# Optimization experiments

Hardware: AMD Instinct MI355X
Metric: run time of the kernel (lower is better)

The kernel has to match this reference:

```python
import jax, jax.numpy as jnp
import numpy as np

N, E, C, S = 30000, 480000, 256, 4
T_EVO = 0.1        # evolution_time
MAX_EIG = 0.5      # max_eigenval in create_ultra_stable_hamiltonian
MAX_NORM = 0.01    # max_norm in ultra_stable_matrix_exp
MAX_TERMS = 4
LN_EPS = 1e-5


def _build_subgraphs(edge_index, n, s):
    """Emulates the per-node k_hop=1 BFS (capped at max_subgraph_size=s) and the
    subgraph laplacian Hamiltonian build (edge_weight=0.1, self-loops added).
    Pure structural preprocessing: integer/constant w.r.t. all float params."""
    src = np.asarray(edge_index[0], dtype=np.int64)
    dst = np.asarray(edge_index[1], dtype=np.int64)
    loops = np.arange(n, dtype=np.int64)
    src = np.concatenate([src, loops]); dst = np.concatenate([dst, loops])
    order = np.argsort(src, kind='stable')
    src_s, dst_s = src[order], dst[order]
    starts = np.searchsorted(src_s, np.arange(n))
    ends = np.searchsorted(src_s, np.arange(n) + 1)
    edge_set = set((src * n + dst).tolist())
    sub_nodes = np.zeros((n, s), dtype=np.int64)
    sub_mask = np.zeros((n, s), dtype=np.float32)
    H = np.zeros((n, s, s), dtype=np.float32)
    for i in range(n):
        nbrs = [i]
        for d in dst_s[starts[i]:ends[i]]:
            d = int(d)
            if d != i and d not in nbrs:
                nbrs.append(d)
                if len(nbrs) == s:
                    break
        m = len(nbrs)
        sub_nodes[i, :m] = nbrs
        sub_nodes[i, m:] = i          # pad with center (masked out below)
        sub_mask[i, :m] = 1.0
        A = np.zeros((s, s), dtype=np.float32)
        for a in range(m):
            ka = nbrs[a] * n
            for b in range(m):
                if (ka + nbrs[b]) in edge_set:
                    A[a, b] = 1.0
        deg = np.maximum(A.sum(axis=1), 1e-6)   # degree(row), clamped like torch
        H[i] = np.diag(deg) - 0.1 * A           # laplacian with edge_weight=0.1
    return sub_nodes, sub_mask, H


def _mat_fro(M):
    return jnp.sqrt(jnp.sum(jnp.abs(M) ** 2, axis=(-2, -1)))


def _unitary_from_H(sub_H):
    """ultra_stable_matrix_exp, batched over N tiny [S,S] Hamiltonians.
    The torch .item() norm/eigenvalue rescales detach gradients, so treating this
    whole block as parameter-independent (it is: H is structural) is faithful."""
    Hc = sub_H.astype(jnp.complex64)
    ev = jnp.linalg.eigvals(Hc)                              # [N,S] (CPU op)
    mx = jnp.max(ev.real, axis=-1)
    Hc = Hc * jnp.where(mx > MAX_EIG, MAX_EIG / mx, 1.0)[:, None, None]
    hn = _mat_fro(Hc)
    Hc = Hc * jnp.where(hn > MAX_NORM, MAX_NORM / hn, 1.0)[:, None, None]
    A = (-1j) * Hc * (T_EVO * 0.1)                           # scaled_H
    I = jnp.eye(S, dtype=jnp.complex64)
    U = jnp.broadcast_to(I, Hc.shape)
    term = U
    for k in range(1, MAX_TERMS + 1):
        term = jnp.matmul(term, A) / k
        tn = _mat_fro(term)
        term = term * jnp.where(tn > 0.1, 0.1 / tn, 1.0)[:, None, None]
        U = U + term
    err = _mat_fro(jnp.matmul(U, jnp.conj(jnp.swapaxes(U, -1, -2))) - I)
    U = jnp.where((err > 0.1)[:, None, None], I + A * 0.01, U)
    return U


def _cplx_linear(xr, xi, wr, wi, br, bi):
    xr = jnp.clip(xr, -10.0, 10.0); xi = jnp.clip(xi, -10.0, 10.0)
    re = xr @ wr.T - xi @ wi.T + br
    im = xr @ wi.T + xi @ wr.T + bi
    return re + 1j * im


def _cln(z, w, b, eps=LN_EPS):
    # UltraStableComplexLayerNorm, training-mode batch stats over dim 0
    mag = jnp.clip(jnp.sqrt(z.real ** 2 + z.imag ** 2 + eps), eps, 1000.0)
    mean = mag.mean(0)
    var = mag.var(0)
    nm = (mag - mean) / (jnp.sqrt(var + eps) + eps)
    sm = jnp.clip(nm * jnp.abs(w) + b, eps, 10.0)
    ph = jnp.arctan2(jnp.clip(z.imag, -1e6, 1e6), jnp.clip(z.real, -1e6, 1e6) + 1e-10)
    return sm * jnp.cos(ph) + 1j * (sm * jnp.sin(ph))


def _crelu(z, leak=0.01, mx=5.0):
    r = jnp.clip(z.real, -mx, mx); i = jnp.clip(z.imag, -mx, mx)
    return jnp.where(r > 0, r, leak * r) + 1j * jnp.where(i > 0, i, leak * i)


def setup_inputs() -> dict:
    key = jax.random.key(0)
    k1, k2, k3, k4 = jax.random.split(key, 4)
    x = jax.random.normal(k1, (N, C), dtype=jnp.float32)
    edge_index = jax.random.randint(k2, (2, E), 0, N, dtype=jnp.int64)
    sub_nodes, sub_mask, sub_H = _build_subgraphs(np.asarray(edge_index), N, S)
    std = np.sqrt(0.5 / C).astype(np.float32)
    w_real = jax.random.normal(k3, (C, C), dtype=jnp.float32) * std
    w_imag = jax.random.normal(k4, (C, C), dtype=jnp.float32) * std
    return {
        'x': x,
        'edge_index': edge_index,
        'sub_nodes': jnp.asarray(sub_nodes),
        'sub_mask': jnp.asarray(sub_mask),
        'sub_H': jnp.asarray(sub_H),
        'w_real': w_real,
        'w_imag': w_imag,
        'b_real': jnp.zeros((C,), jnp.float32),
        'b_imag': jnp.zeros((C,), jnp.float32),
        'ln_weight': jnp.full((C,), 0.1, jnp.float32),
        'ln_bias': jnp.zeros((C,), jnp.float32),
        'evolution_scale': jnp.asarray(0.1, jnp.float32),
    }


def reference(x, edge_index, sub_nodes, sub_mask, sub_H,
              w_real, w_imag, b_real, b_imag, ln_weight, ln_bias,
              evolution_scale):
    # complex linear (input is real -> imag part zero, matching torch.complex(x, 0*x))
    h = _cplx_linear(x, jnp.zeros_like(x), w_real, w_imag, b_real, b_imag)  # [N,C] c64
    U = _unitary_from_H(sub_H)                                              # [N,S,S]
    sub_x = h[sub_nodes] * sub_mask[..., None]                              # [N,S,C]
    # center node is slot 0 of each subgraph -> take row 0 of U @ sub_x
    evolved = jnp.einsum('ns,nsc->nc', U[:, 0, :], sub_x)
    out = evolved * evolution_scale + x.astype(jnp.complex64)  # residual (in==out)
    out = _cln(out, ln_weight, ln_bias)
    out = _crelu(out)
    # dropout is eval-mode identity
    return jnp.concatenate([out.real, out.imag], axis=-1)      # [N, 2C] float32
```

## Files before the change

kernel.cpp:

```cpp
#include <hip/hip_runtime.h>
#include <stdint.h>

#define N_NODES 30000
#define NC 256

typedef _Float16 f16x8 __attribute__((ext_vector_type(8)));
typedef _Float16 f16x4 __attribute__((ext_vector_type(4)));
typedef _Float16 f16x2 __attribute__((ext_vector_type(2)));
typedef float f32x4 __attribute__((ext_vector_type(4)));

#define NBX 7500
#define NBW 128
#define NBP 118
__global__ __launch_bounds__(256) void k_pre(
    const float* __restrict__ x, _Float16* __restrict__ xb,
    const float* __restrict__ wr, const float* __restrict__ wi,
    _Float16* __restrict__ Wb,
    const float* __restrict__ subH, const float* __restrict__ sub_mask,
    const float* __restrict__ escp, float* __restrict__ c4,
    float* __restrict__ ssum, float* __restrict__ ssumsq)
{
    int bid = blockIdx.x, tid = threadIdx.x;
    if (bid < NBX) {
        int i = (bid * 256 + tid) * 4;
        float4 v = *reinterpret_cast<const float4*>(x + i);
        f16x4 o;
        o[0] = (_Float16)fminf(fmaxf(v.x, -10.f), 10.f);
        o[1] = (_Float16)fminf(fmaxf(v.y, -10.f), 10.f);
        o[2] = (_Float16)fminf(fmaxf(v.z, -10.f), 10.f);
        o[3] = (_Float16)fminf(fmaxf(v.w, -10.f), 10.f);
        *reinterpret_cast<f16x4*>(xb + i) = o;
    } else if (bid < NBX + NBW) {
        int i = ((bid - NBX) * 256 + tid) * 4;
        const float* src = (i < NC * NC) ? (wr + i) : (wi + (i - NC * NC));
        float4 v = *reinterpret_cast<const float4*>(src);
        f16x4 o;
        o[0] = (_Float16)v.x; o[1] = (_Float16)v.y;
        o[2] = (_Float16)v.z; o[3] = (_Float16)v.w;
        *reinterpret_cast<f16x4*>(Wb + i) = o;
    } else if (bid < NBX + NBW + NBP) {
        int node = (bid - NBX - NBW) * 256 + tid;
        if (node < N_NODES) {
            float esc = *escp;
            const float4* Hp = reinterpret_cast<const float4*>(subH + node * 16);
            float4 r0 = Hp[0], r1 = Hp[1], r2 = Hp[2], r3 = Hp[3];
            float fr = r0.x * r0.x + r0.y * r0.y + r0.z * r0.z + r0.w * r0.w
                     + r1.x * r1.x + r1.y * r1.y + r1.z * r1.z + r1.w * r1.w
                     + r2.x * r2.x + r2.y * r2.y + r2.z * r2.z + r2.w * r2.w
                     + r3.x * r3.x + r3.y * r3.y + r3.z * r3.z + r3.w * r3.w;
            float coef = 1e-4f * rsqrtf(fr) * esc;
            float4 m = *reinterpret_cast<const float4*>(sub_mask + node * 4);
            float4 o;
            o.x = coef * r0.x * m.x;
            o.y = coef * r0.y * m.y;
            o.z = coef * r0.z * m.z;
            o.w = coef * r0.w * m.w;
            *reinterpret_cast<float4*>(c4 + node * 4) = o;
        }
    } else {
        ssum[tid] = 0.f;
        ssumsq[tid] = 0.f;
    }
}

__global__ __launch_bounds__(256, 2) void k_gemm(
    const _Float16* __restrict__ A, const _Float16* __restrict__ B,
    const float* __restrict__ br, const float* __restrict__ bi,
    _Float16* __restrict__ H)
{
    int bid = blockIdx.x;
    int bm = bid >> 1, cs = bid & 1;
    int tid = threadIdx.x;
    int lane = tid & 63, wave = tid >> 6;
    int quad = lane >> 4, l16 = lane & 15;
    int wm = wave >> 1, wn = wave & 1;
    int row0 = bm * 128 + wm * 64;

    f16x8 af[4][8];
#pragma unroll
    for (int mi = 0; mi < 4; mi++) {
        int r = row0 + mi * 16 + l16;
        if (r >= N_NODES) r = N_NODES - 1;
        const _Float16* ap = A + r * NC + quad * 8;
#pragma unroll
        for (int kc = 0; kc < 8; kc++)
            af[mi][kc] = *reinterpret_cast<const f16x8*>(ap + kc * 32);
    }

    const float* bias_p = wn ? bi : br;
#pragma unroll
    for (int cn = 0; cn < 2; cn++) {
        const _Float16* bbase = B + ((wn ? 256 : 0) + cs * 128 + cn * 64 + l16) * NC
                                  + quad * 8;
        f16x8 bb[2][4];
#pragma unroll
        for (int ni = 0; ni < 4; ni++)
            bb[0][ni] = *reinterpret_cast<const f16x8*>(bbase + ni * 16 * NC);
        f32x4 acc[4][4] = {};
#pragma unroll
        for (int kc = 0; kc < 8; kc++) {
            int cur = kc & 1, nxt = cur ^ 1;
            if (kc < 7) {
#pragma unroll
                for (int ni = 0; ni < 4; ni++)
                    bb[nxt][ni] = *reinterpret_cast<const f16x8*>(
                        bbase + ni * 16 * NC + (kc + 1) * 32);
            }
#pragma unroll
            for (int mi = 0; mi < 4; mi++)
#pragma unroll
                for (int ni = 0; ni < 4; ni++)
                    acc[mi][ni] = __builtin_amdgcn_mfma_f32_16x16x32_f16(
                        af[mi][kc], bb[cur][ni], acc[mi][ni], 0, 0, 0);
        }
#pragma unroll
        for (int ni = 0; ni < 4; ni++) {
            int c = cs * 128 + cn * 64 + ni * 16 + l16;
            float bias = bias_p[c];
            int cc = (wn << 8) + c;
#pragma unroll
            for (int mi = 0; mi < 4; mi++) {
                int rowb = row0 + mi * 16 + quad * 4;
#pragma unroll
                for (int r = 0; r < 4; r++) {
                    int row = rowb + r;
                    if (row < N_NODES)
                        H[row * 512 + cc] = (_Float16)(acc[mi][ni][r] + bias);
                }
            }
        }
    }
}

#define NPB 60
#define NGRP 8
__global__ __launch_bounds__(512) void k_evolve(
    const float* __restrict__ x, const int* __restrict__ sub_nodes,
    const float* __restrict__ c4, const _Float16* __restrict__ h,
    const float* __restrict__ escp,
    float* __restrict__ outz, _Float16* __restrict__ zbuf, int use_f16,
    float* __restrict__ ssum, float* __restrict__ ssumsq)
{
    __shared__ int   s_nodes[NPB][4];
    __shared__ float s_P[NPB][4];
    __shared__ float s_redA[NGRP][256];
    __shared__ float s_redB[NGRP][256];
    int tid = threadIdx.x;
    int g = tid >> 6, lane = tid & 63;
    int base = blockIdx.x * NPB;
    if (tid < NPB) {
        int node = base + tid;
        *reinterpret_cast<float4*>(&s_P[tid][0]) =
            *reinterpret_cast<const float4*>(c4 + node * 4);
        *reinterpret_cast<int4*>(&s_nodes[tid][0]) =
            *reinterpret_cast<const int4*>(sub_nodes + node * 4);
    }
    __syncthreads();
    float esc = *escp;
    float lsum[4] = {0.f, 0.f, 0.f, 0.f};
    float lsq[4]  = {0.f, 0.f, 0.f, 0.f};

    f16x4 hrA[4], hiA[4];
    float4 xA;
    int j = g;
#pragma unroll
    for (int s = 0; s < 4; s++) {
        const _Float16* hp = h + s_nodes[j][s] * 512 + lane * 4;
        hrA[s] = *reinterpret_cast<const f16x4*>(hp);
        hiA[s] = *reinterpret_cast<const f16x4*>(hp + 256);
    }
    xA = *reinterpret_cast<const float4*>(x + (base + j) * NC + lane * 4);

    for (;;) {
        int jn = j + NGRP;
        bool more = jn < NPB;
        f16x4 hrB[4], hiB[4];
        float4 xB;
        if (more) {
#pragma unroll
            for (int s = 0; s < 4; s++) {
                const _Float16* hp = h + s_nodes[jn][s] * 512 + lane * 4;
                hrB[s] = *reinterpret_cast<const f16x4*>(hp);
                hiB[s] = *reinterpret_cast<const f16x4*>(hp + 256);
            }
            xB = *reinterpret_cast<const float4*>(x + (base + jn) * NC + lane * 4);
        }
        {
            int node = base + j;
            float P0 = s_P[j][0], P1 = s_P[j][1], P2 = s_P[j][2], P3 = s_P[j][3];
            float xr[4] = {xA.x, xA.y, xA.z, xA.w};
            f16x8 zo;
            float or4[4], oi4[4];
#pragma unroll
            for (int e = 0; e < 4; e++) {
                float hr0 = (float)hrA[0][e], hi0 = (float)hiA[0][e];
                float hr1 = (float)hrA[1][e], hi1 = (float)hiA[1][e];
                float hr2 = (float)hrA[2][e], hi2 = (float)hiA[2][e];
                float hr3 = (float)hrA[3][e], hi3 = (float)hiA[3][e];
                float er = esc * hr0;
                float ei = esc * hi0;
                er = fmaf(P0, hi0, er); ei = fmaf(-P0, hr0, ei);
                er = fmaf(P1, hi1, er); ei = fmaf(-P1, hr1, ei);
                er = fmaf(P2, hi2, er); ei = fmaf(-P2, hr2, ei);
                er = fmaf(P3, hi3, er); ei = fmaf(-P3, hr3, ei);
                float outr = er + xr[e];
                float outi = ei;
                or4[e] = outr; oi4[e] = outi;
                zo[2 * e] = (_Float16)outr; zo[2 * e + 1] = (_Float16)outi;
                float mag = sqrtf(fmaf(outr, outr, fmaf(outi, outi, 1e-5f)));
                mag = fminf(fmaxf(mag, 1e-5f), 1000.f);
                lsum[e] += mag;
                lsq[e] = fmaf(mag, mag, lsq[e]);
            }
            if (use_f16) {
                *reinterpret_cast<f16x8*>(zbuf + node * 512 + lane * 8) = zo;
            } else {
                *reinterpret_cast<float4*>(outz + node * 512 + lane * 4) =
                    make_float4(or4[0], or4[1], or4[2], or4[3]);
                *reinterpret_cast<float4*>(outz + node * 512 + 256 + lane * 4) =
                    make_float4(oi4[0], oi4[1], oi4[2], oi4[3]);
            }
        }
        if (!more) break;
#pragma unroll
        for (int s = 0; s < 4; s++) { hrA[s] = hrB[s]; hiA[s] = hiB[s]; }
        xA = xB;
        j = jn;
    }
#pragma unroll
    for (int e = 0; e < 4; e++) {
        s_redA[g][lane * 4 + e] = lsum[e];
        s_redB[g][lane * 4 + e] = lsq[e];
    }
    __syncthreads();
    if (tid < 256) {
        float a = 0.f;
#pragma unroll
        for (int q = 0; q < NGRP; q++) a += s_redA[q][tid];
        atomicAdd(&ssum[tid], a);
    } else {
        int t = tid - 256;
        float b = 0.f;
#pragma unroll
        for (int q = 0; q < NGRP; q++) b += s_redB[q][t];
        atomicAdd(&ssumsq[t], b);
    }
}

__global__ __launch_bounds__(256) void k_norm(
    float* __restrict__ out, const _Float16* __restrict__ zbuf, int use_f16,
    const float* __restrict__ ssum, const float* __restrict__ ssumsq,
    const float* __restrict__ lnw, const float* __restrict__ lnb)
{
    int tid = threadIdx.x;
    int node = blockIdx.x * 4 + (tid >> 6);
    int c0 = (tid & 63) * 4;
    float re[4], im[4];
    if (use_f16) {
        f16x8 z = *reinterpret_cast<const f16x8*>(zbuf + node * 512 + c0 * 2);
#pragma unroll
        for (int e = 0; e < 4; e++) { re[e] = (float)z[2 * e]; im[e] = (float)z[2 * e + 1]; }
    } else {
        float4 r4 = *reinterpret_cast<const float4*>(out + node * 512 + c0);
        float4 i4 = *reinterpret_cast<const float4*>(out + node * 512 + 256 + c0);
        re[0] = r4.x; re[1] = r4.y; re[2] = r4.z; re[3] = r4.w;
        im[0] = i4.x; im[1] = i4.y; im[2] = i4.z; im[3] = i4.w;
    }
    float4 s4 = *reinterpret_cast<const float4*>(ssum + c0);
    float4 q4 = *reinterpret_cast<const float4*>(ssumsq + c0);
    float4 w4 = *reinterpret_cast<const float4*>(lnw + c0);
    float4 lb4 = *reinterpret_cast<const float4*>(lnb + c0);
    float S[4] = {s4.x, s4.y, s4.z, s4.w};
    float Q[4] = {q4.x, q4.y, q4.z, q4.w};
    float W[4] = {w4.x, w4.y, w4.z, w4.w};
    float L[4] = {lb4.x, lb4.y, lb4.z, lb4.w};
    const float invN = 1.0f / (float)N_NODES;
    float orr[4], oii[4];
#pragma unroll
    for (int e = 0; e < 4; e++) {
        float mean = S[e] * invN;
        float var = fmaxf(Q[e] * invN - mean * mean, 0.f);
        float denom = sqrtf(var + 1e-5f) + 1e-5f;
        float A = fabsf(W[e]) / denom;
        float Bc = L[e] - mean * A;
        float r = re[e], i = im[e];
        float mag = sqrtf(fmaf(r, r, fmaf(i, i, 1e-5f)));
        mag = fminf(fmaxf(mag, 1e-5f), 1000.f);
        float sm = fmaf(mag, A, Bc);
        sm = fminf(fmaxf(sm, 1e-5f), 10.0f);
        float px = fminf(fmaxf(r, -1e6f), 1e6f) + 1e-10f;
        float py = fminf(fmaxf(i, -1e6f), 1e6f);
        float r2 = fmaf(px, px, py * py);
        float inv = rsqrtf(r2);
        float zr = sm * px * inv, zi = sm * py * inv;
        zr = fminf(fmaxf(zr, -5.f), 5.f);
        zi = fminf(fmaxf(zi, -5.f), 5.f);
        orr[e] = zr > 0.f ? zr : 0.01f * zr;
        oii[e] = zi > 0.f ? zi : 0.01f * zi;
    }
    *reinterpret_cast<float4*>(out + node * 512 + c0) =
        make_float4(orr[0], orr[1], orr[2], orr[3]);
    *reinterpret_cast<float4*>(out + node * 512 + 256 + c0) =
        make_float4(oii[0], oii[1], oii[2], oii[3]);
}

extern "C" void kernel_launch(void* const* d_in, const int* in_sizes, int n_in,
                              void* d_out, int out_size, void* d_ws, size_t ws_size,
                              hipStream_t stream) {
    const float* x        = (const float*)d_in[0];
    const int*   sub_nodes = (const int*)d_in[2];
    const float* sub_mask  = (const float*)d_in[3];
    const float* subH      = (const float*)d_in[4];
    const float* wr  = (const float*)d_in[5];
    const float* wi  = (const float*)d_in[6];
    const float* br  = (const float*)d_in[7];
    const float* bi  = (const float*)d_in[8];
    const float* lnw = (const float*)d_in[9];
    const float* lnb = (const float*)d_in[10];
    const float* esc = (const float*)d_in[11];
    float* out = (float*)d_out;

    char* ws = (char*)d_ws;
    const size_t XB_OFF   = 0;
    const size_t WB_OFF   = 15360000;
    const size_t H_OFF    = 15622144;
    const size_t STAT_OFF = 46342144;
    const size_t C4_OFF   = 46346240;
    const size_t ZB_OFF   = 46826240;
    const size_t WS_NEED_F16 = ZB_OFF + 30720000;
    _Float16* xb = (_Float16*)(ws + XB_OFF);
    _Float16* Wb = (_Float16*)(ws + WB_OFF);
    _Float16* h  = (_Float16*)(ws + H_OFF);
    float* ssum   = (float*)(ws + STAT_OFF);
    float* ssumsq = (float*)(ws + STAT_OFF + 1024);
    float* c4     = (float*)(ws + C4_OFF);
    _Float16* zbuf = (_Float16*)(ws + ZB_OFF);
    int use_f16 = (ws_size >= WS_NEED_F16) ? 1 : 0;

    hipLaunchKernelGGL(k_pre, dim3(NBX + NBW + NBP + 1), dim3(256), 0, stream,
                       x, xb, wr, wi, Wb, subH, sub_mask, esc, c4, ssum, ssumsq);
    hipLaunchKernelGGL(k_gemm, dim3(235 * 2), dim3(256), 0, stream, xb, Wb, br, bi, h);
    hipLaunchKernelGGL(k_evolve, dim3(500), dim3(512), 0, stream,
                       x, sub_nodes, c4, h, esc, out, zbuf, use_f16,
                       ssum, ssumsq);
    hipLaunchKernelGGL(k_norm, dim3(7500), dim3(256), 0, stream,
                       out, zbuf, use_f16, ssum, ssumsq, lnw, lnb);
}
```

Baseline: 194.2 us.

## Retile GEMM to 128x128 per block with streamed double-buffered A/B fragments

The GEMM kernel stops preloading the whole A row-panel into registers (32 f16x8 per thread). Each block now computes a 128x128 output tile, so the grid doubles to four column groups. Both A and B fragments are streamed through two ping-pong register buffers along K, which cuts register pressure enough to raise launch bounds to 3 blocks per SM. The cost is that A is reloaded once per column group, four times instead of twice, and each wave gets less reuse.

```diff
diff --git a/kernel.cpp b/kernel.cpp
--- a/kernel.cpp
+++ b/kernel.cpp
@@ -63,70 +63,96 @@
     }
 }
 
-__global__ __launch_bounds__(256, 2) void k_gemm(
+__global__ __launch_bounds__(256, 3) void k_gemm(
     const _Float16* __restrict__ A, const _Float16* __restrict__ B,
     const float* __restrict__ br, const float* __restrict__ bi,
     _Float16* __restrict__ H)
 {
     int bid = blockIdx.x;
-    int bm = bid >> 1, cs = bid & 1;
+    int bm = bid % 235;
+    int cg = bid / 235;
     int tid = threadIdx.x;
     int lane = tid & 63, wave = tid >> 6;
     int quad = lane >> 4, l16 = lane & 15;
-    int wm = wave >> 1, wn = wave & 1;
+    int wm = wave >> 1, wq = wave & 1;
     int row0 = bm * 128 + wm * 64;
-
-    f16x8 af[4][8];
+    int cbase = cg * 128 + wq * 64;
+
+    const _Float16* ap[4];
 #pragma unroll
     for (int mi = 0; mi < 4; mi++) {
         int r = row0 + mi * 16 + l16;
         if (r >= N_NODES) r = N_NODES - 1;
-        const _Float16* ap = A + r * NC + quad * 8;
-#pragma unroll
-        for (int kc = 0; kc < 8; kc++)
-            af[mi][kc] = *reinterpret_cast<const f16x8*>(ap + kc * 32);
-    }
-
-    const float* bias_p = wn ? bi : br;
-#pragma unroll
-    for (int cn = 0; cn < 2; cn++) {
-        const _Float16* bbase = B + ((wn ? 256 : 0) + cs * 128 + cn * 64 + l16) * NC
-                                  + quad * 8;
-        f16x8 bb[2][4];
-#pragma unroll
-        for (int ni = 0; ni < 4; ni++)
-            bb[0][ni] = *reinterpret_cast<const f16x8*>(bbase + ni * 16 * NC);
-        f32x4 acc[4][4] = {};
-#pragma unroll
-        for (int kc = 0; kc < 8; kc++) {
-            int cur = kc & 1, nxt = cur ^ 1;
-            if (kc < 7) {
-#pragma unroll
-                for (int ni = 0; ni < 4; ni++)
-                    bb[nxt][ni] = *reinterpret_cast<const f16x8*>(
-                        bbase + ni * 16 * NC + (kc + 1) * 32);
+        ap[mi] = A + r * NC + quad * 8;
+    }
+    const _Float16* bp[4];
+#pragma unroll
+    for (int ni = 0; ni < 4; ni++)
+        bp[ni] = B + (cbase + ni * 16 + l16) * NC + quad * 8;
+
+    f16x8 a0[4], a1[4], b0[4], b1[4];
+#pragma unroll
+    for (int i = 0; i < 4; i++) {
+        a0[i] = *reinterpret_cast<const f16x8*>(ap[i]);
+        b0[i] = *reinterpret_cast<const f16x8*>(bp[i]);
+    }
+#pragma unroll
+    for (int i = 0; i < 4; i++) {
+        a1[i] = *reinterpret_cast<const f16x8*>(ap[i] + 32);
+        b1[i] = *reinterpret_cast<const f16x8*>(bp[i] + 32);
+    }
+
+    f32x4 acc[4][4] = {};
+#pragma unroll
+    for (int kc = 0; kc < 8; kc++) {
+        if ((kc & 1) == 0) {
+            if (kc < 6) {
+#pragma unroll
+                for (int i = 0; i < 4; i++) {
+                }
             }
 #pragma unroll
             for (int mi = 0; mi < 4; mi++)
 #pragma unroll
                 for (int ni = 0; ni < 4; ni++)
                     acc[mi][ni] = __builtin_amdgcn_mfma_f32_16x16x32_f16(
-                        af[mi][kc], bb[cur][ni], acc[mi][ni], 0, 0, 0);
-        }
-#pragma unroll
-        for (int ni = 0; ni < 4; ni++) {
-            int c = cs * 128 + cn * 64 + ni * 16 + l16;
-            float bias = bias_p[c];
-            int cc = (wn << 8) + c;
-#pragma unroll
-            for (int mi = 0; mi < 4; mi++) {
-                int rowb = row0 + mi * 16 + quad * 4;
-#pragma unroll
-                for (int r = 0; r < 4; r++) {
-                    int row = rowb + r;
-                    if (row < N_NODES)
-                        H[row * 512 + cc] = (_Float16)(acc[mi][ni][r] + bias);
+                        a0[mi], b0[ni], acc[mi][ni], 0, 0, 0);
+            if (kc < 6) {
+#pragma unroll
+                for (int i = 0; i < 4; i++) {
+                    a0[i] = *reinterpret_cast<const f16x8*>(ap[i] + (kc + 2) * 32);
+                    b0[i] = *reinterpret_cast<const f16x8*>(bp[i] + (kc + 2) * 32);
                 }
+            }
+        } else {
+#pragma unroll
+            for (int mi = 0; mi < 4; mi++)
+#pragma unroll
+                for (int ni = 0; ni < 4; ni++)
+                    acc[mi][ni] = __builtin_amdgcn_mfma_f32_16x16x32_f16(
+                        a1[mi], b1[ni], acc[mi][ni], 0, 0, 0);
+            if (kc < 6) {
+#pragma unroll
+                for (int i = 0; i < 4; i++) {
+                    a1[i] = *reinterpret_cast<const f16x8*>(ap[i] + (kc + 2) * 32);
+                    b1[i] = *reinterpret_cast<const f16x8*>(bp[i] + (kc + 2) * 32);
+                }
+            }
+        }
+    }
+
+#pragma unroll
+    for (int ni = 0; ni < 4; ni++) {
+        int j = cbase + ni * 16 + l16;
+        float bias = (j < 256) ? br[j] : bi[j - 256];
+#pragma unroll
+        for (int mi = 0; mi < 4; mi++) {
+            int rowb = row0 + mi * 16 + quad * 4;
+#pragma unroll
+            for (int r = 0; r < 4; r++) {
+                int row = rowb + r;
+                if (row < N_NODES)
+                    H[row * 512 + j] = (_Float16)(acc[mi][ni][r] + bias);
             }
         }
     }
@@ -339,7 +365,7 @@
 
     hipLaunchKernelGGL(k_pre, dim3(NBX + NBW + NBP + 1), dim3(256), 0, stream,
                        x, xb, wr, wi, Wb, subH, sub_mask, esc, c4, ssum, ssumsq);
-    hipLaunchKernelGGL(k_gemm, dim3(235 * 2), dim3(256), 0, stream, xb, Wb, br, bi, h);
+    hipLaunchKernelGGL(k_gemm, dim3(235 * 4), dim3(256), 0, stream, xb, Wb, br, bi, h);
     hipLaunchKernelGGL(k_evolve, dim3(500), dim3(512), 0, stream,
                        x, sub_nodes, c4, h, esc, out, zbuf, use_f16,
                        ssum, ssumsq);
```

Result: slower. 208.7 us (+7.5%).
